# Optimization experiments

Measured on AMD Instinct MI355X. Metric: run time of the kernel, lower is better.

The kernel has to match this reference:

```python
import jax, jax.numpy as jnp
import numpy as np
from jax import lax

# pywt db4 reconstruction low-pass (scaling) coefficients
_REC_LO = np.array([
    0.23037781330885523, 0.7148465705525415, 0.6308807679295904,
    -0.02798376941698385, -0.18703481171888114, 0.030841381835986965,
    0.032883011666982945, -0.010597401784997278], dtype=np.float64)
_DEC_LO = _REC_LO[::-1].copy()                       # pywt dec_lo = reversed rec_lo
_DEC_HI = (_REC_LO * ((-1.0) ** (np.arange(8) + 1)))  # pywt qmf: dec_hi[k] = (-1)^(k+1) rec_lo[k]
FLEN = 8
LEVEL = 4


def _dwt_level(x):
    """One pywt dwt level, mode='symmetric'. x: [N, n] -> (cA, cD) each [N, floor((n+7)/2)]."""
    # half-sample symmetric extension by FLEN-1 on each side, then drop the first
    # sample so a stride-2 VALID conv lands on pywt's odd-indexed outputs.
    ext = jnp.pad(x, ((0, 0), (FLEN - 1, FLEN - 1)), mode='symmetric')[:, 1:]
    # pywt performs true convolution with dec filters -> flip kernels for XLA correlation
    k = jnp.stack([_DEC_LO[::-1], _DEC_HI[::-1]]).astype(x.dtype)[:, None, :]  # [2,1,8]
    y = lax.conv_general_dilated(ext[:, None, :], k, window_strides=(2,),
                                 padding='VALID',
                                 dimension_numbers=('NCH', 'OIH', 'NCH'))  # [N,2,out]
    return y[:, 0], y[:, 1]


def setup_inputs() -> dict:
    key = jax.random.key(0)
    x = jax.random.normal(key, (64, 32, 8192), dtype=jnp.float32)
    return {"x": x}


def reference(x) -> jnp.ndarray:
    """Batched pywt.wavedec(x, 'db4', mode='symmetric', level=4), coeffs concatenated.
    x: [B, C, L] -> [B, C, wavelet_len] with order [cA4, cD4, cD3, cD2, cD1]."""
    B, C, L = x.shape
    a = x.reshape(B * C, L)
    details = []
    for _ in range(LEVEL):
        a, d = _dwt_level(a)
        details.append(d)
    coeffs = jnp.concatenate([a] + details[::-1], axis=-1)  # [B*C, total]
    return coeffs.reshape(B, C, -1)
```

## Files before the change

kernel.cpp:

```cpp
#include <hip/hip_runtime.h>

#define NT 512

constexpr int L0 = 8192;
constexpr int N1 = 4099;
constexpr int N2 = 2053;
constexpr int N3 = 1030;
constexpr int N4 = 518;
constexpr int ROW_OUT = N4 + N4 + N3 + N2 + N1;
constexpr int OFF_A4 = 0;
constexpr int OFF_D4 = 518;
constexpr int OFF_D3 = 1036;
constexpr int OFF_D2 = 2066;
constexpr int OFF_D1 = 4119;

constexpr int HS = 520;

typedef float f4u __attribute__((ext_vector_type(4), aligned(4)));
typedef float f2u __attribute__((ext_vector_type(2), aligned(4)));

constexpr float GLO[8] = {
    0.23037781330885523f,  0.7148465705525415f,   0.6308807679295904f,
   -0.02798376941698385f, -0.18703481171888114f,  0.030841381835986965f,
    0.032883011666982945f, -0.010597401784997278f };
constexpr float GHI[8] = {
   -0.010597401784997278f, -0.032883011666982945f, 0.030841381835986965f,
    0.18703481171888114f,  -0.02798376941698385f,  -0.6308807679295904f,
    0.7148465705525415f,   -0.23037781330885523f };

__global__ __launch_bounds__(NT, 8) void wavedec4_db4(const float* __restrict__ x,
                                                      float* __restrict__ out)
{
    __shared__ float hA[8 * HS];
    __shared__ float hB[4 * HS];
    const int t = threadIdx.x;
    const float* __restrict__ xr = x + blockIdx.x * (size_t)L0;
    float* __restrict__ outr = out + blockIdx.x * (size_t)ROW_OUT;

    float xw[24];
    if (t > 0) {
        const float4* p = (const float4*)(xr + 16 * t - 8);
        float4 v0 = p[0], v1 = p[1], v2 = p[2], v3 = p[3], v4 = p[4], v5 = p[5];
        xw[0] = v0.x;  xw[1] = v0.y;  xw[2] = v0.z;  xw[3] = v0.w;
        xw[4] = v1.x;  xw[5] = v1.y;  xw[6] = v1.z;  xw[7] = v1.w;
        xw[8] = v2.x;  xw[9] = v2.y;  xw[10] = v2.z; xw[11] = v2.w;
        xw[12] = v3.x; xw[13] = v3.y; xw[14] = v3.z; xw[15] = v3.w;
        xw[16] = v4.x; xw[17] = v4.y; xw[18] = v4.z; xw[19] = v4.w;
        xw[20] = v5.x; xw[21] = v5.y; xw[22] = v5.z; xw[23] = v5.w;
    } else {
        const float4* p = (const float4*)xr;
        float4 v0 = p[0], v1 = p[1], v2 = p[2], v3 = p[3];
        xw[8] = v0.x;  xw[9] = v0.y;  xw[10] = v0.z; xw[11] = v0.w;
        xw[12] = v1.x; xw[13] = v1.y; xw[14] = v1.z; xw[15] = v1.w;
        xw[16] = v2.x; xw[17] = v2.y; xw[18] = v2.z; xw[19] = v2.w;
        xw[20] = v3.x; xw[21] = v3.y; xw[22] = v3.z; xw[23] = v3.w;
#pragma unroll
        for (int k = 0; k < 8; ++k) xw[k] = xw[15 - k];
    }

    float lo1[8], hi1[8];
#pragma unroll
    for (int m = 0; m < 8; ++m) {
        float l = 0.f, h = 0.f;
#pragma unroll
        for (int j = 0; j < 8; ++j) {
            float v = xw[2 * m + 2 + j];
            l = fmaf(GLO[j], v, l);
            h = fmaf(GHI[j], v, h);
        }
        lo1[m] = l;
        hi1[m] = h;
        hA[m * HS + t] = l;
    }
    {
        f4u a = { hi1[0], hi1[1], hi1[2], hi1[3] };
        f4u b = { hi1[4], hi1[5], hi1[6], hi1[7] };
        __builtin_nontemporal_store(a, (f4u*)(outr + OFF_D1 + 8 * t));
        __builtin_nontemporal_store(b, (f4u*)(outr + OFF_D1 + 8 * t + 4));
    }
    if (t == NT - 1) {
#pragma unroll
        for (int e = 0; e < 3; ++e) {
            const int i = 4096 + e;
            float l = 0.f, h = 0.f;
#pragma unroll
            for (int j = 0; j < 8; ++j) {
                int q = 2 * i - 6 + j;
                int idx = ((q <= 8191) ? q : (16383 - q)) - 8168;
                float v = xw[idx];
                l = fmaf(GLO[j], v, l);
                h = fmaf(GHI[j], v, h);
            }
            __builtin_nontemporal_store(h, outr + OFF_D1 + i);
            hA[(i & 7) * HS + (i >> 3)] = l;
        }
    }
    __syncthreads();

    float w2[14];
#pragma unroll
    for (int k = 0; k < 6; ++k) {
        int g = 8 * t - 6 + k;
        if (g < 0) g = -1 - g;
        w2[k] = hA[(g & 7) * HS + (g >> 3)];
    }
#pragma unroll
    for (int m = 0; m < 8; ++m) w2[6 + m] = lo1[m];
    float lo2[4], hi2[4];
#pragma unroll
    for (int m = 0; m < 4; ++m) {
        float l = 0.f, h = 0.f;
#pragma unroll
        for (int j = 0; j < 8; ++j) {
            float v = w2[2 * m + j];
            l = fmaf(GLO[j], v, l);
            h = fmaf(GHI[j], v, h);
        }
        lo2[m] = l;
        hi2[m] = h;
        hB[m * HS + t] = l;
    }
    {
        f4u a = { hi2[0], hi2[1], hi2[2], hi2[3] };
        __builtin_nontemporal_store(a, (f4u*)(outr + OFF_D2 + 4 * t));
    }
    if (t < 5) {
        const int jj = 2048 + t;
        float l = 0.f, h = 0.f;
#pragma unroll
        for (int j = 0; j < 8; ++j) {
            int g = 2 * jj - 6 + j;
            if (g > 4098) g = 8197 - g;
            float v = hA[(g & 7) * HS + (g >> 3)];
            l = fmaf(GLO[j], v, l);
            h = fmaf(GHI[j], v, h);
        }
        __builtin_nontemporal_store(h, outr + OFF_D2 + jj);
        hB[(jj & 3) * HS + (jj >> 2)] = l;
    }
    __syncthreads();

    float w3[10];
#pragma unroll
    for (int k = 0; k < 6; ++k) {
        int g = 4 * t - 6 + k;
        if (g < 0) g = -1 - g;
        w3[k] = hB[(g & 3) * HS + (g >> 2)];
    }
#pragma unroll
    for (int m = 0; m < 4; ++m) w3[6 + m] = lo2[m];
    float lo3[2], hi3[2];
#pragma unroll
    for (int m = 0; m < 2; ++m) {
        float l = 0.f, h = 0.f;
#pragma unroll
        for (int j = 0; j < 8; ++j) {
            float v = w3[2 * m + j];
            l = fmaf(GLO[j], v, l);
            h = fmaf(GHI[j], v, h);
        }
        lo3[m] = l;
        hi3[m] = h;
        hA[m * HS + t] = l;
    }
    {
        f2u a = { hi3[0], hi3[1] };
        __builtin_nontemporal_store(a, (f2u*)(outr + OFF_D3 + 2 * t));
    }
    if (t < 6) {
        const int jj = 1024 + t;
        float l = 0.f, h = 0.f;
#pragma unroll
        for (int j = 0; j < 8; ++j) {
            int g = 2 * jj - 6 + j;
            if (g > 2052) g = 4105 - g;
            float v = hB[(g & 3) * HS + (g >> 2)];
            l = fmaf(GLO[j], v, l);
            h = fmaf(GHI[j], v, h);
        }
        __builtin_nontemporal_store(h, outr + OFF_D3 + jj);
        hA[(jj & 1) * HS + (jj >> 1)] = l;
    }
    __syncthreads();

    float w4[8];
#pragma unroll
    for (int k = 0; k < 6; ++k) {
        int g = 2 * t - 6 + k;
        if (g < 0) g = -1 - g;
        w4[k] = hA[(g & 1) * HS + (g >> 1)];
    }
    w4[6] = lo3[0];
    w4[7] = lo3[1];
    {
        float l = 0.f, h = 0.f;
#pragma unroll
        for (int j = 0; j < 8; ++j) {
            float v = w4[j];
            l = fmaf(GLO[j], v, l);
            h = fmaf(GHI[j], v, h);
        }
        __builtin_nontemporal_store(l, outr + OFF_A4 + t);
        __builtin_nontemporal_store(h, outr + OFF_D4 + t);
    }
    if (t < 6) {
        const int jj = 512 + t;
        float l = 0.f, h = 0.f;
#pragma unroll
        for (int j = 0; j < 8; ++j) {
            int g = 2 * jj - 6 + j;
            if (g > 1029) g = 2059 - g;
            float v = hA[(g & 1) * HS + (g >> 1)];
            l = fmaf(GLO[j], v, l);
            h = fmaf(GHI[j], v, h);
        }
        __builtin_nontemporal_store(l, outr + OFF_A4 + jj);
        __builtin_nontemporal_store(h, outr + OFF_D4 + jj);
    }
}

extern "C" void kernel_launch(void* const* d_in, const int* in_sizes, int n_in,
                              void* d_out, int out_size, void* d_ws, size_t ws_size,
                              hipStream_t stream) {
    const float* x = (const float*)d_in[0];
    float* out = (float*)d_out;
    const int rows = in_sizes[0] / L0;
    wavedec4_db4<<<dim3(rows), dim3(NT), 0, stream>>>(x, out);
}
```

Baseline: 111.7 us.

## Process two rows per block and prefetch the second row's input mid-pipeline

Each block now handles two consecutive rows. The second row's global load is issued during the first row's level-3/4 work so its latency overlaps with compute. Non-temporal stores are also replaced with ordinary stores. The grid is halved, which lowers parallelism and assumes an even row count, and the loaded registers stay live longer.

After: 148.4 us. +32.9%, slower.

```diff
diff --git a/kernel.cpp b/kernel.cpp
--- a/kernel.cpp
+++ b/kernel.cpp
@@ -28,16 +28,9 @@
     0.18703481171888114f,  -0.02798376941698385f,  -0.6308807679295904f,
     0.7148465705525415f,   -0.23037781330885523f };
 
-__global__ __launch_bounds__(NT, 8) void wavedec4_db4(const float* __restrict__ x,
-                                                      float* __restrict__ out)
+__device__ __forceinline__ void load_xw(const float* __restrict__ xr, int t,
+                                        float* __restrict__ xw)
 {
-    __shared__ float hA[8 * HS];
-    __shared__ float hB[4 * HS];
-    const int t = threadIdx.x;
-    const float* __restrict__ xr = x + blockIdx.x * (size_t)L0;
-    float* __restrict__ outr = out + blockIdx.x * (size_t)ROW_OUT;
-
-    float xw[24];
     if (t > 0) {
         const float4* p = (const float4*)(xr + 16 * t - 8);
         float4 v0 = p[0], v1 = p[1], v2 = p[2], v3 = p[3], v4 = p[4], v5 = p[5];
@@ -57,165 +50,185 @@
 #pragma unroll
         for (int k = 0; k < 8; ++k) xw[k] = xw[15 - k];
     }
-
-    float lo1[8], hi1[8];
-#pragma unroll
-    for (int m = 0; m < 8; ++m) {
-        float l = 0.f, h = 0.f;
-#pragma unroll
-        for (int j = 0; j < 8; ++j) {
-            float v = xw[2 * m + 2 + j];
-            l = fmaf(GLO[j], v, l);
-            h = fmaf(GHI[j], v, h);
-        }
-        lo1[m] = l;
-        hi1[m] = h;
-        hA[m * HS + t] = l;
-    }
-    {
-        f4u a = { hi1[0], hi1[1], hi1[2], hi1[3] };
-        f4u b = { hi1[4], hi1[5], hi1[6], hi1[7] };
-        __builtin_nontemporal_store(a, (f4u*)(outr + OFF_D1 + 8 * t));
-        __builtin_nontemporal_store(b, (f4u*)(outr + OFF_D1 + 8 * t + 4));
-    }
-    if (t == NT - 1) {
-#pragma unroll
-        for (int e = 0; e < 3; ++e) {
-            const int i = 4096 + e;
-            float l = 0.f, h = 0.f;
-#pragma unroll
-            for (int j = 0; j < 8; ++j) {
-                int q = 2 * i - 6 + j;
-                int idx = ((q <= 8191) ? q : (16383 - q)) - 8168;
-                float v = xw[idx];
-                l = fmaf(GLO[j], v, l);
-                h = fmaf(GHI[j], v, h);
-            }
-            __builtin_nontemporal_store(h, outr + OFF_D1 + i);
-            hA[(i & 7) * HS + (i >> 3)] = l;
-        }
-    }
-    __syncthreads();
-
-    float w2[14];
-#pragma unroll
-    for (int k = 0; k < 6; ++k) {
-        int g = 8 * t - 6 + k;
-        if (g < 0) g = -1 - g;
-        w2[k] = hA[(g & 7) * HS + (g >> 3)];
-    }
-#pragma unroll
-    for (int m = 0; m < 8; ++m) w2[6 + m] = lo1[m];
-    float lo2[4], hi2[4];
-#pragma unroll
-    for (int m = 0; m < 4; ++m) {
-        float l = 0.f, h = 0.f;
-#pragma unroll
-        for (int j = 0; j < 8; ++j) {
-            float v = w2[2 * m + j];
-            l = fmaf(GLO[j], v, l);
-            h = fmaf(GHI[j], v, h);
-        }
-        lo2[m] = l;
-        hi2[m] = h;
-        hB[m * HS + t] = l;
-    }
-    {
-        f4u a = { hi2[0], hi2[1], hi2[2], hi2[3] };
-        __builtin_nontemporal_store(a, (f4u*)(outr + OFF_D2 + 4 * t));
-    }
-    if (t < 5) {
-        const int jj = 2048 + t;
-        float l = 0.f, h = 0.f;
-#pragma unroll
-        for (int j = 0; j < 8; ++j) {
-            int g = 2 * jj - 6 + j;
-            if (g > 4098) g = 8197 - g;
-            float v = hA[(g & 7) * HS + (g >> 3)];
-            l = fmaf(GLO[j], v, l);
-            h = fmaf(GHI[j], v, h);
-        }
-        __builtin_nontemporal_store(h, outr + OFF_D2 + jj);
-        hB[(jj & 3) * HS + (jj >> 2)] = l;
-    }
-    __syncthreads();
-
-    float w3[10];
-#pragma unroll
-    for (int k = 0; k < 6; ++k) {
-        int g = 4 * t - 6 + k;
-        if (g < 0) g = -1 - g;
-        w3[k] = hB[(g & 3) * HS + (g >> 2)];
-    }
-#pragma unroll
-    for (int m = 0; m < 4; ++m) w3[6 + m] = lo2[m];
-    float lo3[2], hi3[2];
-#pragma unroll
-    for (int m = 0; m < 2; ++m) {
-        float l = 0.f, h = 0.f;
-#pragma unroll
-        for (int j = 0; j < 8; ++j) {
-            float v = w3[2 * m + j];
-            l = fmaf(GLO[j], v, l);
-            h = fmaf(GHI[j], v, h);
-        }
-        lo3[m] = l;
-        hi3[m] = h;
-        hA[m * HS + t] = l;
-    }
-    {
-        f2u a = { hi3[0], hi3[1] };
-        __builtin_nontemporal_store(a, (f2u*)(outr + OFF_D3 + 2 * t));
-    }
-    if (t < 6) {
-        const int jj = 1024 + t;
-        float l = 0.f, h = 0.f;
-#pragma unroll
-        for (int j = 0; j < 8; ++j) {
-            int g = 2 * jj - 6 + j;
-            if (g > 2052) g = 4105 - g;
-            float v = hB[(g & 3) * HS + (g >> 2)];
-            l = fmaf(GLO[j], v, l);
-            h = fmaf(GHI[j], v, h);
-        }
-        __builtin_nontemporal_store(h, outr + OFF_D3 + jj);
-        hA[(jj & 1) * HS + (jj >> 1)] = l;
-    }
-    __syncthreads();
-
-    float w4[8];
-#pragma unroll
-    for (int k = 0; k < 6; ++k) {
-        int g = 2 * t - 6 + k;
-        if (g < 0) g = -1 - g;
-        w4[k] = hA[(g & 1) * HS + (g >> 1)];
-    }
-    w4[6] = lo3[0];
-    w4[7] = lo3[1];
-    {
-        float l = 0.f, h = 0.f;
-#pragma unroll
-        for (int j = 0; j < 8; ++j) {
-            float v = w4[j];
-            l = fmaf(GLO[j], v, l);
-            h = fmaf(GHI[j], v, h);
-        }
-        __builtin_nontemporal_store(l, outr + OFF_A4 + t);
-        __builtin_nontemporal_store(h, outr + OFF_D4 + t);
-    }
-    if (t < 6) {
-        const int jj = 512 + t;
-        float l = 0.f, h = 0.f;
-#pragma unroll
-        for (int j = 0; j < 8; ++j) {
-            int g = 2 * jj - 6 + j;
-            if (g > 1029) g = 2059 - g;
-            float v = hA[(g & 1) * HS + (g >> 1)];
-            l = fmaf(GLO[j], v, l);
-            h = fmaf(GHI[j], v, h);
-        }
-        __builtin_nontemporal_store(l, outr + OFF_A4 + jj);
-        __builtin_nontemporal_store(h, outr + OFF_D4 + jj);
+}
+
+__global__ __launch_bounds__(NT, 8) void wavedec4_db4(const float* __restrict__ x,
+                                                      float* __restrict__ out)
+{
+    __shared__ float hA[8 * HS];
+    __shared__ float hB[4 * HS];
+    const int t = threadIdx.x;
+    const size_t row0 = (size_t)blockIdx.x * 2;
+
+    float xw[24];
+    load_xw(x + row0 * L0, t, xw);
+
+#pragma unroll
+    for (int r = 0; r < 2; ++r) {
+        float* __restrict__ outr = out + (row0 + r) * (size_t)ROW_OUT;
+        if (r == 1) __syncthreads();
+
+        float lo1[8], hi1[8];
+#pragma unroll
+        for (int m = 0; m < 8; ++m) {
+            float l = 0.f, h = 0.f;
+#pragma unroll
+            for (int j = 0; j < 8; ++j) {
+                float v = xw[2 * m + 2 + j];
+                l = fmaf(GLO[j], v, l);
+                h = fmaf(GHI[j], v, h);
+            }
+            lo1[m] = l;
+            hi1[m] = h;
+            hA[m * HS + t] = l;
+        }
+        {
+            f4u a = { hi1[0], hi1[1], hi1[2], hi1[3] };
+            f4u b = { hi1[4], hi1[5], hi1[6], hi1[7] };
+            *(f4u*)(outr + OFF_D1 + 8 * t) = a;
+            *(f4u*)(outr + OFF_D1 + 8 * t + 4) = b;
+        }
+        if (t == NT - 1) {
+#pragma unroll
+            for (int e = 0; e < 3; ++e) {
+                const int i = 4096 + e;
+                float l = 0.f, h = 0.f;
+#pragma unroll
+                for (int j = 0; j < 8; ++j) {
+                    int q = 2 * i - 6 + j;
+                    int idx = ((q <= 8191) ? q : (16383 - q)) - 8168;
+                    float v = xw[idx];
+                    l = fmaf(GLO[j], v, l);
+                    h = fmaf(GHI[j], v, h);
+                }
+                outr[OFF_D1 + i] = h;
+                hA[(i & 7) * HS + (i >> 3)] = l;
+            }
+        }
+        __syncthreads();
+
+        float w2[14];
+#pragma unroll
+        for (int k = 0; k < 6; ++k) {
+            int g = 8 * t - 6 + k;
+            if (g < 0) g = -1 - g;
+            w2[k] = hA[(g & 7) * HS + (g >> 3)];
+        }
+#pragma unroll
+        for (int m = 0; m < 8; ++m) w2[6 + m] = lo1[m];
+        float lo2[4], hi2[4];
+#pragma unroll
+        for (int m = 0; m < 4; ++m) {
+            float l = 0.f, h = 0.f;
+#pragma unroll
+            for (int j = 0; j < 8; ++j) {
+                float v = w2[2 * m + j];
+                l = fmaf(GLO[j], v, l);
+                h = fmaf(GHI[j], v, h);
+            }
+            lo2[m] = l;
+            hi2[m] = h;
+            hB[m * HS + t] = l;
+        }
+        {
+            f4u a = { hi2[0], hi2[1], hi2[2], hi2[3] };
+            *(f4u*)(outr + OFF_D2 + 4 * t) = a;
+        }
+        if (t < 5) {
+            const int jj = 2048 + t;
+            float l = 0.f, h = 0.f;
+#pragma unroll
+            for (int j = 0; j < 8; ++j) {
+                int g = 2 * jj - 6 + j;
+                if (g > 4098) g = 8197 - g;
+                float v = hA[(g & 7) * HS + (g >> 3)];
+                l = fmaf(GLO[j], v, l);
+                h = fmaf(GHI[j], v, h);
+            }
+            outr[OFF_D2 + jj] = h;
+            hB[(jj & 3) * HS + (jj >> 2)] = l;
+        }
+        __syncthreads();
+
+        if (r == 0) load_xw(x + (row0 + 1) * L0, t, xw);
+
+        float w3[10];
+#pragma unroll
+        for (int k = 0; k < 6; ++k) {
+            int g = 4 * t - 6 + k;
+            if (g < 0) g = -1 - g;
+            w3[k] = hB[(g & 3) * HS + (g >> 2)];
+        }
+#pragma unroll
+        for (int m = 0; m < 4; ++m) w3[6 + m] = lo2[m];
+        float lo3[2], hi3[2];
+#pragma unroll
+        for (int m = 0; m < 2; ++m) {
+            float l = 0.f, h = 0.f;
+#pragma unroll
+            for (int j = 0; j < 8; ++j) {
+                float v = w3[2 * m + j];
+                l = fmaf(GLO[j], v, l);
+                h = fmaf(GHI[j], v, h);
+            }
+            lo3[m] = l;
+            hi3[m] = h;
+            hA[m * HS + t] = l;
+        }
+        {
+            f2u a = { hi3[0], hi3[1] };
+            *(f2u*)(outr + OFF_D3 + 2 * t) = a;
+        }
+        if (t < 6) {
+            const int jj = 1024 + t;
+            float l = 0.f, h = 0.f;
+#pragma unroll
+            for (int j = 0; j < 8; ++j) {
+                int g = 2 * jj - 6 + j;
+                if (g > 2052) g = 4105 - g;
+                float v = hB[(g & 3) * HS + (g >> 2)];
+                l = fmaf(GLO[j], v, l);
+                h = fmaf(GHI[j], v, h);
+            }
+            outr[OFF_D3 + jj] = h;
+            hA[(jj & 1) * HS + (jj >> 1)] = l;
+        }
+        __syncthreads();
+
+        float w4[8];
+#pragma unroll
+        for (int k = 0; k < 6; ++k) {
+            int g = 2 * t - 6 + k;
+            if (g < 0) g = -1 - g;
+            w4[k] = hA[(g & 1) * HS + (g >> 1)];
+        }
+        w4[6] = lo3[0];
+        w4[7] = lo3[1];
+        {
+            float l = 0.f, h = 0.f;
+#pragma unroll
+            for (int j = 0; j < 8; ++j) {
+                float v = w4[j];
+                l = fmaf(GLO[j], v, l);
+                h = fmaf(GHI[j], v, h);
+            }
+            outr[OFF_A4 + t] = l;
+            outr[OFF_D4 + t] = h;
+        }
+        if (t < 6) {
+            const int jj = 512 + t;
+            float l = 0.f, h = 0.f;
+#pragma unroll
+            for (int j = 0; j < 8; ++j) {
+                int g = 2 * jj - 6 + j;
+                if (g > 1029) g = 2059 - g;
+                float v = hA[(g & 1) * HS + (g >> 1)];
+                l = fmaf(GLO[j], v, l);
+                h = fmaf(GHI[j], v, h);
+            }
+            outr[OFF_A4 + jj] = l;
+            outr[OFF_D4 + jj] = h;
+        }
     }
 }
 
@@ -225,5 +238,5 @@
     const float* x = (const float*)d_in[0];
     float* out = (float*)d_out;
     const int rows = in_sizes[0] / L0;
-    wavedec4_db4<<<dim3(rows), dim3(NT), 0, stream>>>(x, out);
+    wavedec4_db4<<<dim3(rows / 2), dim3(NT), 0, stream>>>(x, out);
 }
```
